# Optimization experiments

Measured on AMD Instinct MI355X. Metric: run time of the kernel, lower is better.

Reference implementation:

```python
import jax, jax.numpy as jnp
import numpy as np

DEPTH = 10
LEAF = 2 ** DEPTH          # 1024 leaves
NODE_NUM = 2 * LEAF - 1    # 2047
N = NODE_NUM + 1           # 2048 nodes incl. global node 0
ATTN = 4
D = 128
B = 8
L = 2


def _trace_children(ni):
    terms = []
    s, e = ni << 1, (ni << 1) | 1
    while s <= NODE_NUM and e <= NODE_NUM:
        terms.extend(range(s, e + 1))
        s <<= 1
        e = (e << 1) | 1
    return terms


def _trace_left(si):
    ni, cd, terms, stop = si + LEAF, DEPTH, [], False
    while not stop:
        cs = ni - ATTN + 1 - ((ni - ATTN + 1) & 1)
        stop = cs < 2 ** cd
        cs = max(2 ** cd, cs)
        terms.extend(range(cs, ni + 1))
        ni = (cs - 1) >> 1
        cd -= 1
    return terms


def _trace_right(ei):
    ni, cd, terms, stop = ei + LEAF, DEPTH, [], False
    while not stop:
        ce = ni + ATTN - 1 + ((ni - ATTN) & 1)
        stop = ce >= 2 ** (cd + 1)
        ce = min(2 ** (cd + 1) - 1, ce)
        terms.extend(range(ni, ce + 1))
        ni = (ce + 1) >> 1
        cd -= 1
    return terms


def _build_edges():
    src, dst = [], []
    for ni in range(1, NODE_NUM + 1):
        if ni < LEAF:
            t = _trace_children(ni)
        else:
            t = _trace_left(ni - LEAF) + _trace_right(ni - LEAF)
        src.extend(t)
        dst.extend([ni] * len(t))
    e = np.stack([np.asarray(src, np.int64), np.asarray(dst, np.int64)])  # [2, E]
    off = np.arange(B, dtype=np.int64) * N
    eb = (e[:, None, :] + off[None, :, None]).reshape(2, -1)  # batch-offset like _fetch_edge_data
    return eb.astype(np.int32)


def setup_inputs() -> dict:
    key = jax.random.key(0)
    k0, k1, k2 = jax.random.split(key, 3)
    s = 1.0 / np.sqrt(D)
    return {
        "elements": jax.random.normal(k0, (B, LEAF, D), jnp.float32),
        "ln_gamma": jnp.ones((L, D), jnp.float32),
        "ln_beta": jnp.zeros((L, D), jnp.float32),
        "w_nei": (jax.random.normal(k1, (L, D, D), jnp.float32) * s),
        "b_nei": jnp.zeros((L, D), jnp.float32),
        "w_root": (jax.random.normal(k2, (L, D, D), jnp.float32) * s),
        "edge_index": jnp.asarray(_build_edges()),
    }


def _sinusoid(pos, d):
    # ArbitraryPositionEncoder: sinusoidal encoding over (possibly negative) positions
    half = d // 2
    inv = jnp.exp(-jnp.arange(half, dtype=jnp.float32) * (np.log(10000.0) / half))
    ang = pos[:, None] * inv[None, :]  # [n, half]
    return jnp.stack([jnp.sin(ang), jnp.cos(ang)], -1).reshape(pos.shape[0], d)


def reference(elements, ln_gamma, ln_beta, w_nei, b_nei, w_root, edge_index):
    Bx, leaf, d = elements.shape
    depth = int(np.log2(leaf))
    # bottom-up tree compression (mean of two children)
    cur = elements
    levels = [cur]
    for _ in range(depth):
        cur = 0.5 * (cur[:, 0::2] + cur[:, 1::2])
        levels.append(cur)
    # node ordering: [global node 0 (=-1), root (level 0), ..., leaves (level depth)]
    node_feat = jnp.concatenate(
        [jnp.full((Bx, 1, d), -1.0, elements.dtype)] + levels[::-1], axis=1)  # [B, N, D]
    n = node_feat.shape[1]
    # positional encoding: vertical = floor(log2(idx)), horizontal = idx - 2^vertical
    idx = jnp.arange(n, dtype=jnp.float32)
    vpos = jnp.floor(jnp.log2(jnp.where(idx == 0, 0.5, idx)))
    hpos = idx - jnp.exp2(vpos)
    enc = jnp.concatenate([_sinusoid(hpos, d // 2), _sinusoid(vpos, d // 2)], -1)  # [N, D]
    x = (node_feat + enc[None]).reshape(Bx * n, d)
    src, dst = edge_index[0], edge_index[1]
    nseg = Bx * n
    deg = jnp.maximum(
        jax.ops.segment_sum(jnp.ones(src.shape, jnp.float32), dst, num_segments=nseg), 1.0)
    # DeepGCNLayer res+ blocks with SAGEConv (mean aggr)
    for l in range(ln_gamma.shape[0]):
        mu = jnp.mean(x, -1, keepdims=True)
        var = jnp.mean((x - mu) ** 2, -1, keepdims=True)
        h = (x - mu) * jax.lax.rsqrt(var + 1e-5) * ln_gamma[l] + ln_beta[l]
        h = jax.nn.gelu(h, approximate=False)
        agg = jax.ops.segment_sum(h[src], dst, num_segments=nseg) / deg[:, None]
        h = agg @ w_nei[l] + b_nei[l] + h @ w_root[l]
        x = x + h
    return x.reshape(Bx, n, d)
```

## Files before the change

### kernel.cpp

```cpp
#include <hip/hip_runtime.h>
#include <hip/hip_bf16.h>

#define LEAFN 1024
#define NN    2048
#define BATCH 8
#define DD    128
#define ROWS  (BATCH*NN)
#define AHS   384
#define NB    256
#define NT    512

#define LOG1E4_OVER_32 0.28782313662425575f

#define SLACK 9
#define CSTRIDE 136
#define AGGL_OFF 54672
#define RED_OFF  63376

typedef __bf16 bf16x8 __attribute__((ext_vector_type(8)));
typedef float  floatx4 __attribute__((ext_vector_type(4)));
typedef float  floatx2 __attribute__((ext_vector_type(2)));

__device__ __forceinline__ float bf2f(unsigned short u) {
  return __uint_as_float(((unsigned)u) << 16);
}
__device__ __forceinline__ unsigned short f2bf(float f) {
  unsigned u = __float_as_uint(f);
  u += 0x7FFFu + ((u >> 16) & 1u);
  return (unsigned short)(u >> 16);
}
__device__ __forceinline__ float gelu(float v) {
  return 0.5f * v * (1.0f + erff(v * 0.70710678118f));
}
__device__ __forceinline__ floatx2 bfpair(unsigned u) {
  floatx2 r;
  r[0] = __uint_as_float(u << 16);
  r[1] = __uint_as_float(u & 0xffff0000u);
  return r;
}

__device__ __forceinline__ float enc_val(int node, int d) {
  float hp, vp;
  if (node == 0) { hp = -0.5f; vp = -1.0f; }
  else {
    int v = 31 - __clz(node);
    hp = (float)(node - (1 << v));
    vp = (float)v;
  }
  float pos = (d < 64) ? hp : vp;
  int i = ((d < 64) ? d : (d - 64)) >> 1;
  float inv = __expf(-(float)i * LOG1E4_OVER_32);
  float ang = pos * inv;
  return (d & 1) ? __cosf(ang) : __sinf(ang);
}

__device__ __forceinline__ void win_cd(int jb, int cd, int& lo_, int& wd_) {
  int g0 = 1024 + jb * 32, g1 = g0 + 31;
  int a0 = g0 >> (10 - cd), a1 = g1 >> (10 - cd);
  int l = a0 - SLACK, h = a1 + SLACK;
  int lvlo = 1 << cd, lvhi = (2 << cd) - 1;
  lo_ = l < lvlo ? lvlo : l;
  int hh = h > lvhi ? lvhi : h;
  int w = hh - lo_ + 1;
  wd_ = w < 0 ? 0 : w;
}

__device__ __forceinline__ void gbarN(int* bar, int slot) {
  __syncthreads();
  if (threadIdx.x == 0) {
    int g = blockIdx.x & 7;
    int* base = bar + (slot * 8 + g) * 64;
    __threadfence();
    if (__hip_atomic_fetch_add(base, 1, __ATOMIC_RELAXED,
                               __HIP_MEMORY_SCOPE_AGENT) == 31)
      __hip_atomic_store(base + 32, 1, __ATOMIC_RELAXED,
                         __HIP_MEMORY_SCOPE_AGENT);
    while (!__hip_atomic_load(base + 32, __ATOMIC_RELAXED,
                              __HIP_MEMORY_SCOPE_AGENT))
      __builtin_amdgcn_s_sleep(1);
    __threadfence();
  }
  __syncthreads();
}

__device__ __forceinline__ void ph_tree(char* smemc, int b, int s,
                                        const float* __restrict__ elements,
                                        float* __restrict__ x,
                                        float* __restrict__ lvl4,
                                        unsigned short* __restrict__ ah,
                                        const float* __restrict__ gamma,
                                        const float* __restrict__ beta,
                                        float* __restrict__ sroot,
                                        float* xci, int* bar) {
  float* sm = (float*)smemc;
  int tid = threadIdx.x;
  const float4* src = (const float4*)(elements + (size_t)(b * LEAFN + s * 64) * DD);
  for (int i = tid; i < 2048; i += NT) {
    int f = i * 4;
    int j = f >> 7, d = f & 127;
    *(float4*)&sm[(63 + j) * DD + d] = src[i];
  }
  __syncthreads();
  for (int lv = 5; lv >= 0; --lv) {
    int nodes = 1 << lv;
    for (int idx = tid; idx < nodes * DD; idx += NT) {
      int k = nodes + (idx >> 7);
      int d = idx & 127;
      sm[(k - 1) * DD + d] = 0.5f * (sm[(2 * k - 1) * DD + d] + sm[(2 * k) * DD + d]);
    }
    __syncthreads();
  }
  if (tid < DD) lvl4[(b * 16 + s) * DD + tid] = sm[tid];
  __syncthreads();
  if (tid == 0) {
    __threadfence();
    __hip_atomic_store(bar + 1536 + b * 64 + s * 4, 1, __ATOMIC_RELAXED,
                       __HIP_MEMORY_SCOPE_AGENT);
  }
  for (int idx = tid; idx < 127 * DD; idx += NT) {
    int k = (idx >> 7) + 1;
    int d = idx & 127;
    int lv = 31 - __clz(k);
    int g = ((16 + s) << lv) | (k - (1 << lv));
    float xv = sm[idx] + enc_val(g, d);
    if (k >= 64) x[((size_t)(b * NN + g)) * DD + d] = xv;
    sm[idx] = xv;
  }
  __syncthreads();
  {
    int wave = tid >> 6, lane = tid & 63;
    int mt = wave >> 2, nq = wave & 3;
    int m = lane & 15, q = lane >> 4;
#pragma unroll
    for (int c = 0; c < 2; ++c)
#pragma unroll
      for (int ci = 0; ci < 2; ++ci)
#pragma unroll
        for (int r = 0; r < 4; ++r) {
          int t = c * 32 + mt * 16 + q * 4 + r;
          int k = (t == 63) ? 1 : t + 1;
          int d = (nq * 2 + ci) * 16 + m;
          xci[c * 8 + ci * 4 + r] = sm[(k - 1) * DD + d];
        }
  }
  __syncthreads();
  {
    int sub = tid & 7, dp = sub * 16;
    for (int rr = tid >> 3; rr < 127; rr += NT / 8) {
      float* rowp = &sm[rr * DD + dp];
      float4 q0 = *(float4*)rowp;
      float4 q1 = *(float4*)(rowp + 4);
      float4 q2 = *(float4*)(rowp + 8);
      float4 q3 = *(float4*)(rowp + 12);
      float v[16] = {q0.x, q0.y, q0.z, q0.w, q1.x, q1.y, q1.z, q1.w,
                     q2.x, q2.y, q2.z, q2.w, q3.x, q3.y, q3.z, q3.w};
      float s1 = 0.f, s2 = 0.f;
#pragma unroll
      for (int j = 0; j < 16; ++j) { s1 += v[j]; s2 += v[j] * v[j]; }
      s1 += __shfl_xor(s1, 1); s2 += __shfl_xor(s2, 1);
      s1 += __shfl_xor(s1, 2); s2 += __shfl_xor(s2, 2);
      s1 += __shfl_xor(s1, 4); s2 += __shfl_xor(s2, 4);
      float mu = s1 * (1.0f / 128.0f);
      float var = s2 * (1.0f / 128.0f) - mu * mu;
      float rinv = rsqrtf(var + 1e-5f);
      int k = rr + 1, lv = 31 - __clz(k);
      int g = ((16 + s) << lv) | (k - (1 << lv));
      __attribute__((aligned(16))) unsigned short o[16];
      float hv[16];
#pragma unroll
      for (int j = 0; j < 16; ++j) {
        hv[j] = gelu((v[j] - mu) * rinv * gamma[dp + j] + beta[dp + j]);
        o[j] = f2bf(hv[j]);
      }
      *(float4*)rowp        = make_float4(hv[0], hv[1], hv[2], hv[3]);
      *(float4*)(rowp + 4)  = make_float4(hv[4], hv[5], hv[6], hv[7]);
      *(float4*)(rowp + 8)  = make_float4(hv[8], hv[9], hv[10], hv[11]);
      *(float4*)(rowp + 12) = make_float4(hv[12], hv[13], hv[14], hv[15]);
      unsigned short* dst = &ah[(size_t)(b * NN + g) * AHS + 128 + dp];
      *(uint4*)&dst[0] = *(uint4*)&o[0];
      *(uint4*)&dst[8] = *(uint4*)&o[8];
    }
  }
  __syncthreads();
  for (int lv = 5; lv >= 0; --lv) {
    int nk = 1 << lv;
    float inv = 1.0f / (float)((1 << (7 - lv)) - 2);
    for (int idx = tid; idx < nk * DD; idx += NT) {
      int k = nk + (idx >> 7);
      int d = idx & 127;
      float S = sm[(2 * k - 1) * DD + d] + sm[(2 * k) * DD + d];
      if (lv < 5) S += sm[(4 * k - 1) * DD + d] + sm[(4 * k + 1) * DD + d];
      sm[(2 * k - 1) * DD + d] = S;
      int g = ((16 + s) << lv) | (k - nk);
      ah[(size_t)(b * NN + g) * AHS + d] = f2bf(S * inv);
    }
    __syncthreads();
  }
  if (tid < DD) sroot[(size_t)(b * 16 + s) * DD + tid] = sm[DD + tid];
}

__device__ __forceinline__ void ph_top(char* smemc, int b,
                                       const float* __restrict__ lvl4,
                                       unsigned short* __restrict__ ah,
                                       const float* __restrict__ gamma,
                                       const float* __restrict__ beta) {
  float (*xs)[DD] = (float(*)[DD])smemc;
  int tid = threadIdx.x;
  if (tid < 128) {
    int d = tid;
    float v[16];
    for (int j = 0; j < 16; ++j) v[j] = lvl4[(b * 16 + j) * DD + d];
    for (int j = 0; j < 8; ++j) v[j] = 0.5f * (v[2 * j] + v[2 * j + 1]);
    for (int j = 0; j < 8; ++j) xs[8 + j][d] = v[j] + enc_val(8 + j, d);
    for (int j = 0; j < 4; ++j) v[j] = 0.5f * (v[2 * j] + v[2 * j + 1]);
    for (int j = 0; j < 4; ++j) xs[4 + j][d] = v[j] + enc_val(4 + j, d);
    for (int j = 0; j < 2; ++j) v[j] = 0.5f * (v[2 * j] + v[2 * j + 1]);
    for (int j = 0; j < 2; ++j) xs[2 + j][d] = v[j] + enc_val(2 + j, d);
    v[0] = 0.5f * (v[0] + v[1]);
    xs[1][d] = v[0] + enc_val(1, d);
    xs[0][d] = -1.0f + enc_val(0, d);
  }
  __syncthreads();
  if (tid < 128) {
    int rr = tid >> 3, sub = tid & 7, dp = sub * 16;
    float w[16], s1 = 0.f, s2 = 0.f;
#pragma unroll
    for (int j = 0; j < 16; ++j) { w[j] = xs[rr][dp + j]; s1 += w[j]; s2 += w[j] * w[j]; }
    s1 += __shfl_xor(s1, 1); s2 += __shfl_xor(s2, 1);
    s1 += __shfl_xor(s1, 2); s2 += __shfl_xor(s2, 2);
    s1 += __shfl_xor(s1, 4); s2 += __shfl_xor(s2, 4);
    float mu = s1 * (1.0f / 128.0f);
    float var = s2 * (1.0f / 128.0f) - mu * mu;
    float rinv = rsqrtf(var + 1e-5f);
    __attribute__((aligned(16))) unsigned short o[16];
#pragma unroll
    for (int j = 0; j < 16; ++j)
      o[j] = f2bf(gelu((w[j] - mu) * rinv * gamma[dp + j] + beta[dp + j]));
    unsigned short* dst = &ah[(size_t)(b * NN + rr) * AHS + 128 + dp];
    *(uint4*)&dst[0] = *(uint4*)&o[0];
    *(uint4*)&dst[8] = *(uint4*)&o[8];
  }
  __syncthreads();
}

__device__ __forceinline__ void ph_aggsub(char* smemc, int b, int s,
                                          unsigned short* ah,
                                          float* __restrict__ sroot) {
  floatx4 (*S)[32] = (floatx4(*)[32])smemc;
  int tid = threadIdx.x;
  for (int idx = tid; idx < 32 * 32; idx += NT) {
    int k = 32 + (idx >> 5), q = idx & 31;
    int c = (16 + s) * 64 + (2 * k - 64);
    size_t a0 = (size_t)(b * NN + c) * AHS + 256 + q * 4;
    ushort4 u0 = *(const ushort4*)&ah[a0];
    ushort4 u1 = *(const ushort4*)&ah[a0 + AHS];
    floatx4 v;
    v[0] = bf2f(u0.x) + bf2f(u1.x);
    v[1] = bf2f(u0.y) + bf2f(u1.y);
    v[2] = bf2f(u0.z) + bf2f(u1.z);
    v[3] = bf2f(u0.w) + bf2f(u1.w);
    S[k][q] = v;
    int g = (16 + s) * 32 + (k - 32);
    int r = b * NN + g;
    ushort4 o;
    o.x = f2bf(v[0] * 0.5f); o.y = f2bf(v[1] * 0.5f);
    o.z = f2bf(v[2] * 0.5f); o.w = f2bf(v[3] * 0.5f);
    *(ushort4*)&ah[(size_t)r * AHS + q * 4] = o;
  }
  __syncthreads();
  for (int lv = 4; lv >= 0; --lv) {
    int nk = 1 << lv;
    float inv = 1.0f / (float)((1 << (7 - lv)) - 2);
    for (int idx = tid; idx < nk * 32; idx += NT) {
      int k = nk + (idx >> 5), q = idx & 31;
      int c = ((16 + s) << (lv + 1)) | (2 * k - 2 * nk);
      size_t a0 = (size_t)(b * NN + c) * AHS + 256 + q * 4;
      ushort4 u0 = *(const ushort4*)&ah[a0];
      ushort4 u1 = *(const ushort4*)&ah[a0 + AHS];
      floatx4 sc0 = S[2 * k][q], sc1 = S[2 * k + 1][q];
      floatx4 v;
      v[0] = bf2f(u0.x) + bf2f(u1.x) + sc0[0] + sc1[0];
      v[1] = bf2f(u0.y) + bf2f(u1.y) + sc0[1] + sc1[1];
      v[2] = bf2f(u0.z) + bf2f(u1.z) + sc0[2] + sc1[2];
      v[3] = bf2f(u0.w) + bf2f(u1.w) + sc0[3] + sc1[3];
      S[k][q] = v;
      int g = ((16 + s) << lv) | (k - nk);
      int r = b * NN + g;
      ushort4 o;
      o.x = f2bf(v[0] * inv); o.y = f2bf(v[1] * inv);
      o.z = f2bf(v[2] * inv); o.w = f2bf(v[3] * inv);
      *(ushort4*)&ah[(size_t)r * AHS + q * 4] = o;
    }
    __syncthreads();
  }
  for (int q = tid; q < 32; q += NT)
    ((floatx4*)sroot)[(size_t)(b * 16 + s) * 32 + q] = S[1][q];
}

__device__ __forceinline__ void ph_leafagg(char* smemc, int b, int jb,
                                           const int* __restrict__ srcv,
                                           const int* __restrict__ s0a,
                                           const int* __restrict__ s1a,
                                           const unsigned short* __restrict__ eoff,
                                           unsigned short* ah, int hoff) {
  unsigned short* cache = (unsigned short*)smemc;
  int tid = threadIdx.x;
  int lo[11], wd[11], off[11];
  int acc_off = 0;
#pragma unroll
  for (int cd = 10; cd >= 1; --cd) {
    win_cd(jb, cd, lo[cd], wd[cd]);
    off[cd] = acc_off;
    acc_off += wd[cd];
  }
#pragma unroll
  for (int cd = 10; cd >= 1; --cd) {
    int w = wd[cd];
    for (int t = tid; t < w * 16; t += NT) {
      int row = t >> 4, seg = t & 15;
      *(uint4*)&cache[(off[cd] + row) * CSTRIDE + seg * 8] =
          *(const uint4*)&ah[(size_t)(b * NN + lo[cd] + row) * AHS + hoff + seg * 8];
    }
  }
  __syncthreads();

  int leaf = tid >> 4, c = tid & 15;
  int r = b * NN + 1024 + jb * 32 + leaf;
  int e0 = s0a[r], e1 = s1a[r];
  int cb = c * 16;
  floatx2 a0 = {0.f, 0.f}, a1 = {0.f, 0.f}, a2 = {0.f, 0.f}, a3 = {0.f, 0.f};
  auto one = [&](int ei) {
    unsigned o = eoff[ei];
    uint4 u;
    if (o != 0xFFFFu)
      u = *(const uint4*)(smemc + o + cb);
    else {
      int g = srcv[ei] - b * NN;
      u = *(const uint4*)&ah[(size_t)(b * NN + g) * AHS + hoff + c * 8];
    }
    a0 += bfpair(u.x); a1 += bfpair(u.y); a2 += bfpair(u.z); a3 += bfpair(u.w);
  };
  int e = e0;
  for (; e + 4 <= e1; e += 4) {
    unsigned o0 = eoff[e], o1 = eoff[e + 1], o2 = eoff[e + 2], o3 = eoff[e + 3];
    if (!((((o0 + 1) | (o1 + 1) | (o2 + 1) | (o3 + 1)) >> 16))) {
      uint4 u0 = *(const uint4*)(smemc + o0 + cb);
      uint4 u1 = *(const uint4*)(smemc + o1 + cb);
      uint4 u2 = *(const uint4*)(smemc + o2 + cb);
      uint4 u3 = *(const uint4*)(smemc + o3 + cb);
      a0 += bfpair(u0.x); a1 += bfpair(u0.y); a2 += bfpair(u0.z); a3 += bfpair(u0.w);
      a0 += bfpair(u1.x); a1 += bfpair(u1.y); a2 += bfpair(u1.z); a3 += bfpair(u1.w);
      a0 += bfpair(u2.x); a1 += bfpair(u2.y); a2 += bfpair(u2.z); a3 += bfpair(u2.w);
      a0 += bfpair(u3.x); a1 += bfpair(u3.y); a2 += bfpair(u3.z); a3 += bfpair(u3.w);
    } else {
      one(e); one(e + 1); one(e + 2); one(e + 3);
    }
  }
  for (; e < e1; ++e) one(e);
  float inv = 1.0f / (float)max(e1 - e0, 1);
  unsigned short* aggl = (unsigned short*)(smemc + AGGL_OFF);
  __attribute__((aligned(16))) unsigned short o[8];
  o[0] = f2bf(a0[0] * inv); o[1] = f2bf(a0[1] * inv);
  o[2] = f2bf(a1[0] * inv); o[3] = f2bf(a1[1] * inv);
  o[4] = f2bf(a2[0] * inv); o[5] = f2bf(a2[1] * inv);
  o[6] = f2bf(a3[0] * inv); o[7] = f2bf(a3[1] * inv);
  *(uint4*)&aggl[leaf * CSTRIDE + c * 8] = *(uint4*)&o[0];
}

__device__ __forceinline__ void ph_topfin(int b,
                                          const float* __restrict__ sroot,
                                          unsigned short* ah, int hoff) {
  int d = threadIdx.x;
  float S16[16], h16[16], Sv[16];
#pragma unroll
  for (int j = 0; j < 16; ++j) S16[j] = sroot[(size_t)(b * 16 + j) * DD + d];
#pragma unroll
  for (int j = 0; j < 16; ++j)
    h16[j] = bf2f(ah[(size_t)(b * NN + 16 + j) * AHS + hoff + d]);
#pragma unroll
  for (int k = 8; k < 16; ++k)
    Sv[k] = h16[2 * k - 16] + h16[2 * k - 15] + S16[2 * k - 16] + S16[2 * k - 15];
#pragma unroll
  for (int k = 7; k >= 1; --k)
    Sv[k] = bf2f(ah[(size_t)(b * NN + 2 * k) * AHS + hoff + d]) +
            bf2f(ah[(size_t)(b * NN + 2 * k + 1) * AHS + hoff + d]) +
            Sv[2 * k] + Sv[2 * k + 1];
#pragma unroll
  for (int k = 1; k < 16; ++k) {
    int dv = 31 - __clz(k);
    float inv = 1.0f / (float)((1 << (11 - dv)) - 2);
    ah[(size_t)(b * NN + k) * AHS + d] = f2bf(Sv[k] * inv);
  }
  ah[(size_t)(b * NN) * AHS + d] = f2bf(0.0f);
}

__device__ __forceinline__ void ph_gemm32(char* redc, const unsigned short* aggl,
                                          int rowbase, unsigned short* ah,
                                          const unsigned short* __restrict__ wfl,
                                          const float* __restrict__ bn,
                                          float* __restrict__ x, int hoff_in,
                                          const float* __restrict__ gamma,
                                          const float* __restrict__ beta,
                                          float* xc, int first_layer) {
  int wave = threadIdx.x >> 6, lane = threadIdx.x & 63;
  int mt = wave >> 2, nq = wave & 3;
  int r0 = rowbase + mt * 16;
  int m = lane & 15, q = lane >> 4;
  const unsigned short* arow = ah + (size_t)(r0 + m) * AHS + q * 8;
  const bf16x8* B = (const bf16x8*)wfl + lane;
  floatx4 acc[2];
  acc[0] = (floatx4){0.f, 0.f, 0.f, 0.f};
  acc[1] = (floatx4){0.f, 0.f, 0.f, 0.f};
#pragma unroll
  for (int kc = 0; kc < 8; ++kc) {
    bf16x8 a0;
    if (kc < 4)
      a0 = *(const bf16x8*)&aggl[(mt * 16 + m) * CSTRIDE + kc * 32 + q * 8];
    else
      a0 = *(const bf16x8*)(arow + hoff_in + (kc - 4) * 32);
#pragma unroll
    for (int ci = 0; ci < 2; ++ci) {
      bf16x8 bb = B[(kc * 8 + nq * 2 + ci) * 64];
      acc[ci] = __builtin_amdgcn_mfma_f32_16x16x32_bf16(a0, bb, acc[ci], 0, 0, 0);
    }
  }
  if (first_layer) {
    float s1[4] = {0.f, 0.f, 0.f, 0.f}, s2[4] = {0.f, 0.f, 0.f, 0.f};
#pragma unroll
    for (int ci = 0; ci < 2; ++ci) {
      int col = (nq * 2 + ci) * 16 + m;
      float bias = bn[col];
#pragma unroll
      for (int r = 0; r < 4; ++r) {
        int row = r0 + q * 4 + r;
        float v = x[(size_t)row * DD + col] + acc[ci][r] + bias;
        xc[ci * 4 + r] = v;
        s1[r] += v; s2[r] += v * v;
      }
    }
#pragma unroll
    for (int r = 0; r < 4; ++r) {
      s1[r] += __shfl_xor(s1[r], 1); s2[r] += __shfl_xor(s2[r], 1);
      s1[r] += __shfl_xor(s1[r], 2); s2[r] += __shfl_xor(s2[r], 2);
      s1[r] += __shfl_xor(s1[r], 4); s2[r] += __shfl_xor(s2[r], 4);
      s1[r] += __shfl_xor(s1[r], 8); s2[r] += __shfl_xor(s2[r], 8);
    }
    float* red = (float*)redc;
    int rl = mt * 16 + q * 4;
    __syncthreads();
    if (m == 0) {
#pragma unroll
      for (int r = 0; r < 4; ++r) {
        red[(rl + r) * 4 + nq] = s1[r];
        red[128 + (rl + r) * 4 + nq] = s2[r];
      }
    }
    __syncthreads();
    float mu[4], rv[4];
#pragma unroll
    for (int r = 0; r < 4; ++r) {
      float t1 = red[(rl + r) * 4] + red[(rl + r) * 4 + 1] +
                 red[(rl + r) * 4 + 2] + red[(rl + r) * 4 + 3];
      float t2 = red[128 + (rl + r) * 4] + red[128 + (rl + r) * 4 + 1] +
                 red[128 + (rl + r) * 4 + 2] + red[128 + (rl + r) * 4 + 3];
      mu[r] = t1 * (1.0f / 128.0f);
      float var = t2 * (1.0f / 128.0f) - mu[r] * mu[r];
      rv[r] = rsqrtf(var + 1e-5f);
    }
#pragma unroll
    for (int ci = 0; ci < 2; ++ci) {
      int col = (nq * 2 + ci) * 16 + m;
      float gm = gamma[col], bt = beta[col];
#pragma unroll
      for (int r = 0; r < 4; ++r) {
        int row = r0 + q * 4 + r;
        float hh = gelu((xc[ci * 4 + r] - mu[r]) * rv[r] * gm + bt);
        ah[(size_t)row * AHS + 256 + col] = f2bf(hh);
      }
    }
  } else {
#pragma unroll
    for (int ci = 0; ci < 2; ++ci) {
      int col = (nq * 2 + ci) * 16 + m;
      float bias = bn[col];
#pragma unroll
      for (int r = 0; r < 4; ++r) {
        int row = r0 + q * 4 + r;
        x[(size_t)row * DD + col] = xc[ci * 4 + r] + acc[ci][r] + bias;
      }
    }
  }
}

__device__ __forceinline__ void ph_gemm32s(char* redc, int b, int sb, int tbase,
                                           unsigned short* ah,
                                           const unsigned short* __restrict__ wfl,
                                           const float* __restrict__ bn,
                                           float* __restrict__ x, int hoff_in,
                                           const float* __restrict__ gamma,
                                           const float* __restrict__ beta,
                                           float* xc, int first_layer) {
  int wave = threadIdx.x >> 6, lane = threadIdx.x & 63;
  int mt = wave >> 2, nq = wave & 3;
  int m = lane & 15, q = lane >> 4;
  int tA = tbase + mt * 16 + m;
  int kA = (tA == 63) ? 1 : tA + 1;
  int lvA = 31 - __clz(kA);
  int rowA = b * NN + (((16 + sb) << lvA) | (kA - (1 << lvA)));
  int rowO[4];
#pragma unroll
  for (int r = 0; r < 4; ++r) {
    int t = tbase + mt * 16 + q * 4 + r;
    int k = (t == 63) ? 1 : t + 1;
    int lv = 31 - __clz(k);
    rowO[r] = b * NN + (((16 + sb) << lv) | (k - (1 << lv)));
  }
  const unsigned short* arow = ah + (size_t)rowA * AHS + q * 8;
  const bf16x8* B = (const bf16x8*)wfl + lane;
  floatx4 acc[2];
  acc[0] = (floatx4){0.f, 0.f, 0.f, 0.f};
  acc[1] = (floatx4){0.f, 0.f, 0.f, 0.f};
#pragma unroll
  for (int kc = 0; kc < 8; ++kc) {
    int koff = (kc < 4) ? kc * 32 : hoff_in + (kc - 4) * 32;
    bf16x8 a0 = *(const bf16x8*)(arow + koff);
#pragma unroll
    for (int ci = 0; ci < 2; ++ci) {
      bf16x8 bb = B[(kc * 8 + nq * 2 + ci) * 64];
      acc[ci] = __builtin_amdgcn_mfma_f32_16x16x32_bf16(a0, bb, acc[ci], 0, 0, 0);
    }
  }
  if (first_layer) {
    float s1[4] = {0.f, 0.f, 0.f, 0.f}, s2[4] = {0.f, 0.f, 0.f, 0.f};
#pragma unroll
    for (int ci = 0; ci < 2; ++ci) {
      int col = (nq * 2 + ci) * 16 + m;
      float bias = bn[col];
#pragma unroll
      for (int r = 0; r < 4; ++r) {
        float v = xc[ci * 4 + r] + acc[ci][r] + bias;
        xc[ci * 4 + r] = v;
        s1[r] += v; s2[r] += v * v;
      }
    }
#pragma unroll
    for (int r = 0; r < 4; ++r) {
      s1[r] += __shfl_xor(s1[r], 1); s2[r] += __shfl_xor(s2[r], 1);
      s1[r] += __shfl_xor(s1[r], 2); s2[r] += __shfl_xor(s2[r], 2);
      s1[r] += __shfl_xor(s1[r], 4); s2[r] += __shfl_xor(s2[r], 4);
      s1[r] += __shfl_xor(s1[r], 8); s2[r] += __shfl_xor(s2[r], 8);
    }
    float* red = (float*)redc;
    int rl = mt * 16 + q * 4;
    __syncthreads();
    if (m == 0) {
#pragma unroll
      for (int r = 0; r < 4; ++r) {
        red[(rl + r) * 4 + nq] = s1[r];
        red[128 + (rl + r) * 4 + nq] = s2[r];
      }
    }
    __syncthreads();
    float mu[4], rv[4];
#pragma unroll
    for (int r = 0; r < 4; ++r) {
      float t1 = red[(rl + r) * 4] + red[(rl + r) * 4 + 1] +
                 red[(rl + r) * 4 + 2] + red[(rl + r) * 4 + 3];
      float t2 = red[128 + (rl + r) * 4] + red[128 + (rl + r) * 4 + 1] +
                 red[128 + (rl + r) * 4 + 2] + red[128 + (rl + r) * 4 + 3];
      mu[r] = t1 * (1.0f / 128.0f);
      float var = t2 * (1.0f / 128.0f) - mu[r] * mu[r];
      rv[r] = rsqrtf(var + 1e-5f);
    }
#pragma unroll
    for (int ci = 0; ci < 2; ++ci) {
      int col = (nq * 2 + ci) * 16 + m;
      float gm = gamma[col], bt = beta[col];
#pragma unroll
      for (int r = 0; r < 4; ++r) {
        float hh = gelu((xc[ci * 4 + r] - mu[r]) * rv[r] * gm + bt);
        ah[(size_t)rowO[r] * AHS + 256 + col] = f2bf(hh);
      }
    }
  } else {
#pragma unroll
    for (int ci = 0; ci < 2; ++ci) {
      int col = (nq * 2 + ci) * 16 + m;
      float bias = bn[col];
#pragma unroll
      for (int r = 0; r < 4; ++r)
        x[(size_t)rowO[r] * DD + col] = xc[ci * 4 + r] + acc[ci][r] + bias;
    }
  }
}

__device__ __forceinline__ void ph_gemm16t(char* redc, int b,
                                           unsigned short* ah,
                                           const unsigned short* __restrict__ wfl,
                                           const float* __restrict__ bn,
                                           float* __restrict__ x, int hoff_in,
                                           const float* __restrict__ gamma,
                                           const float* __restrict__ beta,
                                           float* xc, int first_layer) {
  int ct = threadIdx.x >> 6, lane = threadIdx.x & 63;
  int m = lane & 15, q = lane >> 4;
  const unsigned short* arow = ah + (size_t)(b * NN + m) * AHS + q * 8;
  const bf16x8* B = (const bf16x8*)wfl + lane;
  floatx4 acc = (floatx4){0.f, 0.f, 0.f, 0.f};
#pragma unroll
  for (int kc = 0; kc < 8; ++kc) {
    int koff = (kc < 4) ? kc * 32 : hoff_in + (kc - 4) * 32;
    bf16x8 a0 = *(const bf16x8*)(arow + koff);
    bf16x8 bb = B[(kc * 8 + ct) * 64];
    acc = __builtin_amdgcn_mfma_f32_16x16x32_bf16(a0, bb, acc, 0, 0, 0);
  }
  int col = ct * 16 + m;
  float bias = bn[col];
  if (first_layer) {
    float s1[4], s2[4];
#pragma unroll
    for (int r = 0; r < 4; ++r) {
      float v = xc[r] + acc[r] + bias;
      xc[r] = v; s1[r] = v; s2[r] = v * v;
    }
#pragma unroll
    for (int r = 0; r < 4; ++r) {
      s1[r] += __shfl_xor(s1[r], 1); s2[r] += __shfl_xor(s2[r], 1);
      s1[r] += __shfl_xor(s1[r], 2); s2[r] += __shfl_xor(s2[r], 2);
      s1[r] += __shfl_xor(s1[r], 4); s2[r] += __shfl_xor(s2[r], 4);
      s1[r] += __shfl_xor(s1[r], 8); s2[r] += __shfl_xor(s2[r], 8);
    }
    float* red = (float*)redc;
    __syncthreads();
    if (m == 0) {
#pragma unroll
      for (int r = 0; r < 4; ++r) {
        red[(q * 4 + r) * 8 + ct] = s1[r];
        red[128 + (q * 4 + r) * 8 + ct] = s2[r];
      }
    }
    __syncthreads();
#pragma unroll
    for (int r = 0; r < 4; ++r) {
      float t1 = 0.f, t2 = 0.f;
#pragma unroll
      for (int j = 0; j < 8; ++j) {
        t1 += red[(q * 4 + r) * 8 + j];
        t2 += red[128 + (q * 4 + r) * 8 + j];
      }
      float mu = t1 * (1.0f / 128.0f);
      float var = t2 * (1.0f / 128.0f) - mu * mu;
      float rv = rsqrtf(var + 1e-5f);
      float hh = gelu((xc[r] - mu) * rv * gamma[col] + beta[col]);
      ah[(size_t)(b * NN + q * 4 + r) * AHS + 256 + col] = f2bf(hh);
    }
  } else {
#pragma unroll
    for (int r = 0; r < 4; ++r)
      x[(size_t)(b * NN + q * 4 + r) * DD + col] = xc[r] + acc[r] + bias;
  }
}

__global__ __launch_bounds__(NT, 1) void k_mega(
    const float* __restrict__ elements, const float* __restrict__ ln_gamma,
    const float* __restrict__ ln_beta, const float* __restrict__ w_nei,
    const float* __restrict__ b_nei, const float* __restrict__ w_root,
    const int* __restrict__ srcv, const int* __restrict__ dstv, int E,
    float* __restrict__ x, int* s0a, int* s1a, float* lvl4, float* sroot,
    unsigned short* wf, unsigned short* ah, unsigned short* eoff, int* bar) {
  __shared__ __align__(16) char smem[65536];
  int bid = blockIdx.x, tid = threadIdx.x;
  int b = bid & 7, gb = bid >> 3;
  int Eb = E >> 3;
  unsigned short* wfg = wf + (size_t)b * 65536;
  float xcl[8], xci[16], xct[4];

  if (gb < 16) {
    ph_tree(smem, b, gb, elements, x, lvl4, ah, ln_gamma, ln_beta, sroot, xci, bar);
  } else if (gb < 24) {
    int base = b * Eb;
    for (int i = base + (gb - 16) * NT + tid; i < base + Eb; i += 8 * NT) {
      int dv = dstv[i];
      if (i == 0 || dstv[i - 1] != dv) s0a[dv] = i;
      if (i == base + Eb - 1 || dstv[i + 1] != dv) s1a[dv] = i + 1;
    }
    for (int i = base + (gb - 16) * NT + tid; i < base + Eb; i += 8 * NT) {
      int dl = dstv[i] - b * NN - 1024;
      unsigned short ov = 0xFFFFu;
      if (dl >= 0) {
        int jb2 = dl >> 5;
        int g = srcv[i] - b * NN;
        int lv = 31 - __clz(g);
        int acc2 = 0;
#pragma unroll
        for (int cd = 10; cd >= 1; --cd) {
          int lo_, wd_;
          win_cd(jb2, cd, lo_, wd_);
          if (cd == lv) {
            int idx = g - lo_;
            if ((unsigned)idx < (unsigned)wd_)
              ov = (unsigned short)((acc2 + idx) * (2 * CSTRIDE));
          }
          acc2 += wd_;
        }
      }
      eoff[i] = ov;
    }
    if (gb == 16) {
      if (tid < 16) {
        while (!__hip_atomic_load(bar + 1536 + b * 64 + tid * 4, __ATOMIC_RELAXED,
                                  __HIP_MEMORY_SCOPE_AGENT))
          __builtin_amdgcn_s_sleep(1);
        __threadfence();
      }
      __syncthreads();
      ph_top(smem, b, lvl4, ah, ln_gamma, ln_beta);
      {
        int wv = tid >> 6, ln = tid & 63, m_ = ln & 15, q_ = ln >> 4;
        float (*xs)[DD] = (float(*)[DD])smem;
#pragma unroll
        for (int r = 0; r < 4; ++r) xct[r] = xs[q_ * 4 + r][wv * 16 + m_];
      }
    }
  } else {
    int gi = (gb - 24) * NT + tid;
    int lane = gi & 63, ct = (gi >> 6) & 7, kc = gi >> 9;
    int n = ct * 16 + (lane & 15);
    int k = kc * 32 + (lane >> 4) * 8;
    int kk = k & 127;
#pragma unroll
    for (int l = 0; l < 2; ++l) {
      const float* w = (k < 128) ? (w_nei + (size_t)l * DD * DD)
                                 : (w_root + (size_t)l * DD * DD);
      unsigned short* o = wfg + (size_t)l * 32768 + (size_t)gi * 8;
#pragma unroll
      for (int j = 0; j < 8; ++j) o[j] = f2bf(w[(size_t)(kk + j) * DD + n]);
    }
  }
  gbarN(bar, 0);

  if (gb == 16) {
    if (tid < 128) ph_topfin(b, sroot, ah, 128);
    __syncthreads();
    ph_gemm16t(smem + RED_OFF, b, ah, wfg, b_nei, x, 128,
               ln_gamma + DD, ln_beta + DD, xct, 1);
    __syncthreads();
  }
  ph_leafagg(smem, b, gb, srcv, s0a, s1a, eoff, ah, 128);
  __syncthreads();
  ph_gemm32(smem + RED_OFF, (const unsigned short*)(smem + AGGL_OFF),
            b * NN + 1024 + gb * 32, ah, wfg, b_nei, x, 128,
            ln_gamma + DD, ln_beta + DD, xcl, 1);
  if (gb < 16) {
    ph_gemm32s(smem + RED_OFF, b, gb, 0, ah, wfg, b_nei, x, 128,
               ln_gamma + DD, ln_beta + DD, xci, 1);
    ph_gemm32s(smem + RED_OFF, b, gb, 32, ah, wfg, b_nei, x, 128,
               ln_gamma + DD, ln_beta + DD, xci + 8, 1);
  }
  gbarN(bar, 1);

  if (gb < 16) {
    ph_aggsub(smem, b, gb, ah, sroot);
    __syncthreads();
    if (tid == 0) {
      __threadfence();
      __hip_atomic_store(bar + 1024 + b * 64 + gb * 4, 1, __ATOMIC_RELAXED,
                         __HIP_MEMORY_SCOPE_AGENT);
    }
  }
  ph_leafagg(smem, b, gb, srcv, s0a, s1a, eoff, ah, 256);
  __syncthreads();
  ph_gemm32(smem + RED_OFF, (const unsigned short*)(smem + AGGL_OFF),
            b * NN + 1024 + gb * 32, ah, wfg + 32768, b_nei + DD,
            x, 256, ln_gamma, ln_beta, xcl, 0);
  if (gb < 16) {
    ph_gemm32s(smem + RED_OFF, b, gb, 0, ah, wfg + 32768, b_nei + DD, x, 256,
               ln_gamma, ln_beta, xci, 0);
    ph_gemm32s(smem + RED_OFF, b, gb, 32, ah, wfg + 32768, b_nei + DD, x, 256,
               ln_gamma, ln_beta, xci + 8, 0);
  } else if (gb == 16) {
    if (tid < 16) {
      while (!__hip_atomic_load(bar + 1024 + b * 64 + tid * 4, __ATOMIC_RELAXED,
                                __HIP_MEMORY_SCOPE_AGENT))
        __builtin_amdgcn_s_sleep(1);
      __threadfence();
    }
    __syncthreads();
    if (tid < 128) ph_topfin(b, sroot, ah, 256);
    __syncthreads();
    ph_gemm16t(smem + RED_OFF, b, ah, wfg + 32768, b_nei + DD, x, 256,
               ln_gamma, ln_beta, xct, 0);
  }
}

extern "C" void kernel_launch(void* const* d_in, const int* in_sizes, int n_in,
                              void* d_out, int out_size, void* d_ws, size_t ws_size,
                              hipStream_t stream) {
  const float* elements = (const float*)d_in[0];
  const float* ln_gamma = (const float*)d_in[1];
  const float* ln_beta  = (const float*)d_in[2];
  const float* w_nei    = (const float*)d_in[3];
  const float* b_nei    = (const float*)d_in[4];
  const float* w_root   = (const float*)d_in[5];
  const int*   edge     = (const int*)d_in[6];
  int E = in_sizes[6] / 2;
  const int* srcv = edge;
  const int* dstv = edge + E;
  float* x = (float*)d_out;

  char* ws = (char*)d_ws;
  int*            bar   = (int*)ws;
  int*            s0    = (int*)(ws + 65536);
  int*            s1    = (int*)(ws + 131072);
  float*          lvl4  = (float*)(ws + 196608);
  float*          sroot = (float*)(ws + 262144);
  unsigned short* wf    = (unsigned short*)(ws + 327680);
  unsigned short* ah    = (unsigned short*)(ws + 327680 + 1048576);
  unsigned short* eoff  = (unsigned short*)(ws + 327680 + 1048576 + 12582912);

  hipMemsetAsync(bar, 0, 8192, stream);
  k_mega<<<dim3(NB), dim3(NT), 0, stream>>>(
      elements, ln_gamma, ln_beta, w_nei, b_nei, w_root,
      srcv, dstv, E, x, s0, s1, lvl4, sroot, wf, ah, eoff, bar);
}
```

Before: 175.0 us.

## Double block threads to 1024 and split leaf edge aggregation across two half-groups

Raises threads per block from 512 to 1024 in the persistent mega-kernel. Leaf aggregation now gives each leaf two 16-lane groups that each sum half of its edge list and combine the halves with a shuffle. The MFMA GEMM phases keep only the first 8 waves active and guard the extra waves. The aim is more latency hiding in the gather-heavy aggregation, at the risk of halving the register budget per thread and adding idle waves that still pay at every block barrier.

New measurement: 169.0 us. 3.5% less time.

```diff
diff --git a/kernel.cpp b/kernel.cpp
--- a/kernel.cpp
+++ b/kernel.cpp
@@ -8,7 +8,7 @@
 #define ROWS  (BATCH*NN)
 #define AHS   384
 #define NB    256
-#define NT    512
+#define NT    1024
 
 #define LOG1E4_OVER_32 0.28782313662425575f
 
@@ -129,19 +129,21 @@
   __syncthreads();
   {
     int wave = tid >> 6, lane = tid & 63;
-    int mt = wave >> 2, nq = wave & 3;
-    int m = lane & 15, q = lane >> 4;
-#pragma unroll
-    for (int c = 0; c < 2; ++c)
-#pragma unroll
-      for (int ci = 0; ci < 2; ++ci)
-#pragma unroll
-        for (int r = 0; r < 4; ++r) {
-          int t = c * 32 + mt * 16 + q * 4 + r;
-          int k = (t == 63) ? 1 : t + 1;
-          int d = (nq * 2 + ci) * 16 + m;
-          xci[c * 8 + ci * 4 + r] = sm[(k - 1) * DD + d];
-        }
+    if (wave < 8) {
+      int mt = wave >> 2, nq = wave & 3;
+      int m = lane & 15, q = lane >> 4;
+#pragma unroll
+      for (int c = 0; c < 2; ++c)
+#pragma unroll
+        for (int ci = 0; ci < 2; ++ci)
+#pragma unroll
+          for (int r = 0; r < 4; ++r) {
+            int t = c * 32 + mt * 16 + q * 4 + r;
+            int k = (t == 63) ? 1 : t + 1;
+            int d = (nq * 2 + ci) * 16 + m;
+            xci[c * 8 + ci * 4 + r] = sm[(k - 1) * DD + d];
+          }
+    }
   }
   __syncthreads();
   {
@@ -324,9 +326,13 @@
   }
   __syncthreads();
 
-  int leaf = tid >> 4, c = tid & 15;
+  int leaf = tid >> 5, half = (tid >> 4) & 1, c = tid & 15;
   int r = b * NN + 1024 + jb * 32 + leaf;
   int e0 = s0a[r], e1 = s1a[r];
+  int n = e1 - e0;
+  int mid = e0 + (n >> 1);
+  int ebeg = half ? mid : e0;
+  int eend = half ? e1 : mid;
   int cb = c * 16;
   floatx2 a0 = {0.f, 0.f}, a1 = {0.f, 0.f}, a2 = {0.f, 0.f}, a3 = {0.f, 0.f};
   auto one = [&](int ei) {
@@ -340,8 +346,8 @@
     }
     a0 += bfpair(u.x); a1 += bfpair(u.y); a2 += bfpair(u.z); a3 += bfpair(u.w);
   };
-  int e = e0;
-  for (; e + 4 <= e1; e += 4) {
+  int e = ebeg;
+  for (; e + 4 <= eend; e += 4) {
     unsigned o0 = eoff[e], o1 = eoff[e + 1], o2 = eoff[e + 2], o3 = eoff[e + 3];
     if (!((((o0 + 1) | (o1 + 1) | (o2 + 1) | (o3 + 1)) >> 16))) {
       uint4 u0 = *(const uint4*)(smemc + o0 + cb);
@@ -356,15 +362,21 @@
       one(e); one(e + 1); one(e + 2); one(e + 3);
     }
   }
-  for (; e < e1; ++e) one(e);
-  float inv = 1.0f / (float)max(e1 - e0, 1);
-  unsigned short* aggl = (unsigned short*)(smemc + AGGL_OFF);
-  __attribute__((aligned(16))) unsigned short o[8];
-  o[0] = f2bf(a0[0] * inv); o[1] = f2bf(a0[1] * inv);
-  o[2] = f2bf(a1[0] * inv); o[3] = f2bf(a1[1] * inv);
-  o[4] = f2bf(a2[0] * inv); o[5] = f2bf(a2[1] * inv);
-  o[6] = f2bf(a3[0] * inv); o[7] = f2bf(a3[1] * inv);
-  *(uint4*)&aggl[leaf * CSTRIDE + c * 8] = *(uint4*)&o[0];
+  for (; e < eend; ++e) one(e);
+  a0[0] += __shfl_xor(a0[0], 16); a0[1] += __shfl_xor(a0[1], 16);
+  a1[0] += __shfl_xor(a1[0], 16); a1[1] += __shfl_xor(a1[1], 16);
+  a2[0] += __shfl_xor(a2[0], 16); a2[1] += __shfl_xor(a2[1], 16);
+  a3[0] += __shfl_xor(a3[0], 16); a3[1] += __shfl_xor(a3[1], 16);
+  if (!half) {
+    float inv = 1.0f / (float)max(n, 1);
+    unsigned short* aggl = (unsigned short*)(smemc + AGGL_OFF);
+    __attribute__((aligned(16))) unsigned short o[8];
+    o[0] = f2bf(a0[0] * inv); o[1] = f2bf(a0[1] * inv);
+    o[2] = f2bf(a1[0] * inv); o[3] = f2bf(a1[1] * inv);
+    o[4] = f2bf(a2[0] * inv); o[5] = f2bf(a2[1] * inv);
+    o[6] = f2bf(a3[0] * inv); o[7] = f2bf(a3[1] * inv);
+    *(uint4*)&aggl[leaf * CSTRIDE + c * 8] = *(uint4*)&o[0];
+  }
 }
 
 __device__ __forceinline__ void ph_topfin(int b,
@@ -403,52 +415,57 @@
                                           const float* __restrict__ beta,
                                           float* xc, int first_layer) {
   int wave = threadIdx.x >> 6, lane = threadIdx.x & 63;
-  int mt = wave >> 2, nq = wave & 3;
+  bool act = wave < 8;
+  int mt = (wave & 7) >> 2, nq = wave & 3;
   int r0 = rowbase + mt * 16;
   int m = lane & 15, q = lane >> 4;
-  const unsigned short* arow = ah + (size_t)(r0 + m) * AHS + q * 8;
-  const bf16x8* B = (const bf16x8*)wfl + lane;
   floatx4 acc[2];
   acc[0] = (floatx4){0.f, 0.f, 0.f, 0.f};
   acc[1] = (floatx4){0.f, 0.f, 0.f, 0.f};
-#pragma unroll
-  for (int kc = 0; kc < 8; ++kc) {
-    bf16x8 a0;
-    if (kc < 4)
-      a0 = *(const bf16x8*)&aggl[(mt * 16 + m) * CSTRIDE + kc * 32 + q * 8];
-    else
-      a0 = *(const bf16x8*)(arow + hoff_in + (kc - 4) * 32);
-#pragma unroll
-    for (int ci = 0; ci < 2; ++ci) {
-      bf16x8 bb = B[(kc * 8 + nq * 2 + ci) * 64];
-      acc[ci] = __builtin_amdgcn_mfma_f32_16x16x32_bf16(a0, bb, acc[ci], 0, 0, 0);
+  if (act) {
+    const unsigned short* arow = ah + (size_t)(r0 + m) * AHS + q * 8;
+    const bf16x8* B = (const bf16x8*)wfl + lane;
+#pragma unroll
+    for (int kc = 0; kc < 8; ++kc) {
+      bf16x8 a0;
+      if (kc < 4)
+        a0 = *(const bf16x8*)&aggl[(mt * 16 + m) * CSTRIDE + kc * 32 + q * 8];
+      else
+        a0 = *(const bf16x8*)(arow + hoff_in + (kc - 4) * 32);
+#pragma unroll
+      for (int ci = 0; ci < 2; ++ci) {
+        bf16x8 bb = B[(kc * 8 + nq * 2 + ci) * 64];
+        acc[ci] = __builtin_amdgcn_mfma_f32_16x16x32_bf16(a0, bb, acc[ci], 0, 0, 0);
+      }
     }
   }
   if (first_layer) {
     float s1[4] = {0.f, 0.f, 0.f, 0.f}, s2[4] = {0.f, 0.f, 0.f, 0.f};
-#pragma unroll
-    for (int ci = 0; ci < 2; ++ci) {
-      int col = (nq * 2 + ci) * 16 + m;
-      float bias = bn[col];
-#pragma unroll
-      for (int r = 0; r < 4; ++r) {
-        int row = r0 + q * 4 + r;
-        float v = x[(size_t)row * DD + col] + acc[ci][r] + bias;
-        xc[ci * 4 + r] = v;
-        s1[r] += v; s2[r] += v * v;
-      }
-    }
-#pragma unroll
-    for (int r = 0; r < 4; ++r) {
-      s1[r] += __shfl_xor(s1[r], 1); s2[r] += __shfl_xor(s2[r], 1);
-      s1[r] += __shfl_xor(s1[r], 2); s2[r] += __shfl_xor(s2[r], 2);
-      s1[r] += __shfl_xor(s1[r], 4); s2[r] += __shfl_xor(s2[r], 4);
-      s1[r] += __shfl_xor(s1[r], 8); s2[r] += __shfl_xor(s2[r], 8);
+    if (act) {
+#pragma unroll
+      for (int ci = 0; ci < 2; ++ci) {
+        int col = (nq * 2 + ci) * 16 + m;
+        float bias = bn[col];
+#pragma unroll
+        for (int r = 0; r < 4; ++r) {
+          int row = r0 + q * 4 + r;
+          float v = x[(size_t)row * DD + col] + acc[ci][r] + bias;
+          xc[ci * 4 + r] = v;
+          s1[r] += v; s2[r] += v * v;
+        }
+      }
+#pragma unroll
+      for (int r = 0; r < 4; ++r) {
+        s1[r] += __shfl_xor(s1[r], 1); s2[r] += __shfl_xor(s2[r], 1);
+        s1[r] += __shfl_xor(s1[r], 2); s2[r] += __shfl_xor(s2[r], 2);
+        s1[r] += __shfl_xor(s1[r], 4); s2[r] += __shfl_xor(s2[r], 4);
+        s1[r] += __shfl_xor(s1[r], 8); s2[r] += __shfl_xor(s2[r], 8);
+      }
     }
     float* red = (float*)redc;
     int rl = mt * 16 + q * 4;
     __syncthreads();
-    if (m == 0) {
+    if (act && m == 0) {
 #pragma unroll
       for (int r = 0; r < 4; ++r) {
         red[(rl + r) * 4 + nq] = s1[r];
@@ -456,37 +473,41 @@
       }
     }
     __syncthreads();
-    float mu[4], rv[4];
-#pragma unroll
-    for (int r = 0; r < 4; ++r) {
-      float t1 = red[(rl + r) * 4] + red[(rl + r) * 4 + 1] +
-                 red[(rl + r) * 4 + 2] + red[(rl + r) * 4 + 3];
-      float t2 = red[128 + (rl + r) * 4] + red[128 + (rl + r) * 4 + 1] +
-                 red[128 + (rl + r) * 4 + 2] + red[128 + (rl + r) * 4 + 3];
-      mu[r] = t1 * (1.0f / 128.0f);
-      float var = t2 * (1.0f / 128.0f) - mu[r] * mu[r];
-      rv[r] = rsqrtf(var + 1e-5f);
-    }
-#pragma unroll
-    for (int ci = 0; ci < 2; ++ci) {
-      int col = (nq * 2 + ci) * 16 + m;
-      float gm = gamma[col], bt = beta[col];
-#pragma unroll
-      for (int r = 0; r < 4; ++r) {
-        int row = r0 + q * 4 + r;
-        float hh = gelu((xc[ci * 4 + r] - mu[r]) * rv[r] * gm + bt);
-        ah[(size_t)row * AHS + 256 + col] = f2bf(hh);
+    if (act) {
+      float mu[4], rv[4];
+#pragma unroll
+      for (int r = 0; r < 4; ++r) {
+        float t1 = red[(rl + r) * 4] + red[(rl + r) * 4 + 1] +
+                   red[(rl + r) * 4 + 2] + red[(rl + r) * 4 + 3];
+        float t2 = red[128 + (rl + r) * 4] + red[128 + (rl + r) * 4 + 1] +
+                   red[128 + (rl + r) * 4 + 2] + red[128 + (rl + r) * 4 + 3];
+        mu[r] = t1 * (1.0f / 128.0f);
+        float var = t2 * (1.0f / 128.0f) - mu[r] * mu[r];
+        rv[r] = rsqrtf(var + 1e-5f);
+      }
+#pragma unroll
+      for (int ci = 0; ci < 2; ++ci) {
+        int col = (nq * 2 + ci) * 16 + m;
+        float gm = gamma[col], bt = beta[col];
+#pragma unroll
+        for (int r = 0; r < 4; ++r) {
+          int row = r0 + q * 4 + r;
+          float hh = gelu((xc[ci * 4 + r] - mu[r]) * rv[r] * gm + bt);
+          ah[(size_t)row * AHS + 256 + col] = f2bf(hh);
+        }
       }
     }
   } else {
-#pragma unroll
-    for (int ci = 0; ci < 2; ++ci) {
-      int col = (nq * 2 + ci) * 16 + m;
-      float bias = bn[col];
-#pragma unroll
-      for (int r = 0; r < 4; ++r) {
-        int row = r0 + q * 4 + r;
-        x[(size_t)row * DD + col] = xc[ci * 4 + r] + acc[ci][r] + bias;
+    if (act) {
+#pragma unroll
+      for (int ci = 0; ci < 2; ++ci) {
+        int col = (nq * 2 + ci) * 16 + m;
+        float bias = bn[col];
+#pragma unroll
+        for (int r = 0; r < 4; ++r) {
+          int row = r0 + q * 4 + r;
+          x[(size_t)row * DD + col] = xc[ci * 4 + r] + acc[ci][r] + bias;
+        }
       }
     }
   }
@@ -501,7 +522,8 @@
                                            const float* __restrict__ beta,
                                            float* xc, int first_layer) {
   int wave = threadIdx.x >> 6, lane = threadIdx.x & 63;
-  int mt = wave >> 2, nq = wave & 3;
+  bool act = wave < 8;
+  int mt = (wave & 7) >> 2, nq = wave & 3;
   int m = lane & 15, q = lane >> 4;
   int tA = tbase + mt * 16 + m;
   int kA = (tA == 63) ? 1 : tA + 1;
@@ -515,45 +537,49 @@
     int lv = 31 - __clz(k);
     rowO[r] = b * NN + (((16 + sb) << lv) | (k - (1 << lv)));
   }
-  const unsigned short* arow = ah + (size_t)rowA * AHS + q * 8;
-  const bf16x8* B = (const bf16x8*)wfl + lane;
   floatx4 acc[2];
   acc[0] = (floatx4){0.f, 0.f, 0.f, 0.f};
   acc[1] = (floatx4){0.f, 0.f, 0.f, 0.f};
-#pragma unroll
-  for (int kc = 0; kc < 8; ++kc) {
-    int koff = (kc < 4) ? kc * 32 : hoff_in + (kc - 4) * 32;
-    bf16x8 a0 = *(const bf16x8*)(arow + koff);
-#pragma unroll
-    for (int ci = 0; ci < 2; ++ci) {
-      bf16x8 bb = B[(kc * 8 + nq * 2 + ci) * 64];
-      acc[ci] = __builtin_amdgcn_mfma_f32_16x16x32_bf16(a0, bb, acc[ci], 0, 0, 0);
+  if (act) {
+    const unsigned short* arow = ah + (size_t)rowA * AHS + q * 8;
+    const bf16x8* B = (const bf16x8*)wfl + lane;
+#pragma unroll
+    for (int kc = 0; kc < 8; ++kc) {
+      int koff = (kc < 4) ? kc * 32 : hoff_in + (kc - 4) * 32;
+      bf16x8 a0 = *(const bf16x8*)(arow + koff);
+#pragma unroll
+      for (int ci = 0; ci < 2; ++ci) {
+        bf16x8 bb = B[(kc * 8 + nq * 2 + ci) * 64];
+        acc[ci] = __builtin_amdgcn_mfma_f32_16x16x32_bf16(a0, bb, acc[ci], 0, 0, 0);
+      }
     }
   }
   if (first_layer) {
     float s1[4] = {0.f, 0.f, 0.f, 0.f}, s2[4] = {0.f, 0.f, 0.f, 0.f};
-#pragma unroll
-    for (int ci = 0; ci < 2; ++ci) {
-      int col = (nq * 2 + ci) * 16 + m;
-      float bias = bn[col];
-#pragma unroll
-      for (int r = 0; r < 4; ++r) {
-        float v = xc[ci * 4 + r] + acc[ci][r] + bias;
-        xc[ci * 4 + r] = v;
-        s1[r] += v; s2[r] += v * v;
-      }
-    }
-#pragma unroll
-    for (int r = 0; r < 4; ++r) {
-      s1[r] += __shfl_xor(s1[r], 1); s2[r] += __shfl_xor(s2[r], 1);
-      s1[r] += __shfl_xor(s1[r], 2); s2[r] += __shfl_xor(s2[r], 2);
-      s1[r] += __shfl_xor(s1[r], 4); s2[r] += __shfl_xor(s2[r], 4);
-      s1[r] += __shfl_xor(s1[r], 8); s2[r] += __shfl_xor(s2[r], 8);
+    if (act) {
+#pragma unroll
+      for (int ci = 0; ci < 2; ++ci) {
+        int col = (nq * 2 + ci) * 16 + m;
+        float bias = bn[col];
+#pragma unroll
+        for (int r = 0; r < 4; ++r) {
+          float v = xc[ci * 4 + r] + acc[ci][r] + bias;
+          xc[ci * 4 + r] = v;
+          s1[r] += v; s2[r] += v * v;
+        }
+      }
+#pragma unroll
+      for (int r = 0; r < 4; ++r) {
+        s1[r] += __shfl_xor(s1[r], 1); s2[r] += __shfl_xor(s2[r], 1);
+        s1[r] += __shfl_xor(s1[r], 2); s2[r] += __shfl_xor(s2[r], 2);
+        s1[r] += __shfl_xor(s1[r], 4); s2[r] += __shfl_xor(s2[r], 4);
+        s1[r] += __shfl_xor(s1[r], 8); s2[r] += __shfl_xor(s2[r], 8);
+      }
     }
     float* red = (float*)redc;
     int rl = mt * 16 + q * 4;
     __syncthreads();
-    if (m == 0) {
+    if (act && m == 0) {
 #pragma unroll
       for (int r = 0; r < 4; ++r) {
         red[(rl + r) * 4 + nq] = s1[r];
@@ -561,35 +587,39 @@
       }
     }
     __syncthreads();
-    float mu[4], rv[4];
-#pragma unroll
-    for (int r = 0; r < 4; ++r) {
-      float t1 = red[(rl + r) * 4] + red[(rl + r) * 4 + 1] +
-                 red[(rl + r) * 4 + 2] + red[(rl + r) * 4 + 3];
-      float t2 = red[128 + (rl + r) * 4] + red[128 + (rl + r) * 4 + 1] +
-                 red[128 + (rl + r) * 4 + 2] + red[128 + (rl + r) * 4 + 3];
-      mu[r] = t1 * (1.0f / 128.0f);
-      float var = t2 * (1.0f / 128.0f) - mu[r] * mu[r];
-      rv[r] = rsqrtf(var + 1e-5f);
-    }
-#pragma unroll
-    for (int ci = 0; ci < 2; ++ci) {
-      int col = (nq * 2 + ci) * 16 + m;
-      float gm = gamma[col], bt = beta[col];
-#pragma unroll
-      for (int r = 0; r < 4; ++r) {
-        float hh = gelu((xc[ci * 4 + r] - mu[r]) * rv[r] * gm + bt);
-        ah[(size_t)rowO[r] * AHS + 256 + col] = f2bf(hh);
+    if (act) {
+      float mu[4], rv[4];
+#pragma unroll
+      for (int r = 0; r < 4; ++r) {
+        float t1 = red[(rl + r) * 4] + red[(rl + r) * 4 + 1] +
+                   red[(rl + r) * 4 + 2] + red[(rl + r) * 4 + 3];
+        float t2 = red[128 + (rl + r) * 4] + red[128 + (rl + r) * 4 + 1] +
+                   red[128 + (rl + r) * 4 + 2] + red[128 + (rl + r) * 4 + 3];
+        mu[r] = t1 * (1.0f / 128.0f);
+        float var = t2 * (1.0f / 128.0f) - mu[r] * mu[r];
+        rv[r] = rsqrtf(var + 1e-5f);
+      }
+#pragma unroll
+      for (int ci = 0; ci < 2; ++ci) {
+        int col = (nq * 2 + ci) * 16 + m;
+        float gm = gamma[col], bt = beta[col];
+#pragma unroll
+        for (int r = 0; r < 4; ++r) {
+          float hh = gelu((xc[ci * 4 + r] - mu[r]) * rv[r] * gm + bt);
+          ah[(size_t)rowO[r] * AHS + 256 + col] = f2bf(hh);
+        }
       }
     }
   } else {
-#pragma unroll
-    for (int ci = 0; ci < 2; ++ci) {
-      int col = (nq * 2 + ci) * 16 + m;
-      float bias = bn[col];
-#pragma unroll
-      for (int r = 0; r < 4; ++r)
-        x[(size_t)rowO[r] * DD + col] = xc[ci * 4 + r] + acc[ci][r] + bias;
+    if (act) {
+#pragma unroll
+      for (int ci = 0; ci < 2; ++ci) {
+        int col = (nq * 2 + ci) * 16 + m;
+        float bias = bn[col];
+#pragma unroll
+        for (int r = 0; r < 4; ++r)
+          x[(size_t)rowO[r] * DD + col] = xc[ci * 4 + r] + acc[ci][r] + bias;
+      }
     }
   }
 }
@@ -603,36 +633,41 @@
                                            const float* __restrict__ beta,
                                            float* xc, int first_layer) {
   int ct = threadIdx.x >> 6, lane = threadIdx.x & 63;
+  bool act = ct < 8;
   int m = lane & 15, q = lane >> 4;
-  const unsigned short* arow = ah + (size_t)(b * NN + m) * AHS + q * 8;
-  const bf16x8* B = (const bf16x8*)wfl + lane;
   floatx4 acc = (floatx4){0.f, 0.f, 0.f, 0.f};
-#pragma unroll
-  for (int kc = 0; kc < 8; ++kc) {
-    int koff = (kc < 4) ? kc * 32 : hoff_in + (kc - 4) * 32;
-    bf16x8 a0 = *(const bf16x8*)(arow + koff);
-    bf16x8 bb = B[(kc * 8 + ct) * 64];
-    acc = __builtin_amdgcn_mfma_f32_16x16x32_bf16(a0, bb, acc, 0, 0, 0);
-  }
-  int col = ct * 16 + m;
-  float bias = bn[col];
+  int col = (ct & 7) * 16 + m;
+  if (act) {
+    const unsigned short* arow = ah + (size_t)(b * NN + m) * AHS + q * 8;
+    const bf16x8* B = (const bf16x8*)wfl + lane;
+#pragma unroll
+    for (int kc = 0; kc < 8; ++kc) {
+      int koff = (kc < 4) ? kc * 32 : hoff_in + (kc - 4) * 32;
+      bf16x8 a0 = *(const bf16x8*)(arow + koff);
+      bf16x8 bb = B[(kc * 8 + ct) * 64];
+      acc = __builtin_amdgcn_mfma_f32_16x16x32_bf16(a0, bb, acc, 0, 0, 0);
+    }
+  }
   if (first_layer) {
-    float s1[4], s2[4];
-#pragma unroll
-    for (int r = 0; r < 4; ++r) {
-      float v = xc[r] + acc[r] + bias;
-      xc[r] = v; s1[r] = v; s2[r] = v * v;
-    }
-#pragma unroll
-    for (int r = 0; r < 4; ++r) {
-      s1[r] += __shfl_xor(s1[r], 1); s2[r] += __shfl_xor(s2[r], 1);
-      s1[r] += __shfl_xor(s1[r], 2); s2[r] += __shfl_xor(s2[r], 2);
-      s1[r] += __shfl_xor(s1[r], 4); s2[r] += __shfl_xor(s2[r], 4);
-      s1[r] += __shfl_xor(s1[r], 8); s2[r] += __shfl_xor(s2[r], 8);
+    float s1[4] = {0.f, 0.f, 0.f, 0.f}, s2[4] = {0.f, 0.f, 0.f, 0.f};
+    float bias = act ? bn[col] : 0.f;
+    if (act) {
+#pragma unroll
+      for (int r = 0; r < 4; ++r) {
+        float v = xc[r] + acc[r] + bias;
+        xc[r] = v; s1[r] = v; s2[r] = v * v;
+      }
+#pragma unroll
+      for (int r = 0; r < 4; ++r) {
+        s1[r] += __shfl_xor(s1[r], 1); s2[r] += __shfl_xor(s2[r], 1);
+        s1[r] += __shfl_xor(s1[r], 2); s2[r] += __shfl_xor(s2[r], 2);
+        s1[r] += __shfl_xor(s1[r], 4); s2[r] += __shfl_xor(s2[r], 4);
+        s1[r] += __shfl_xor(s1[r], 8); s2[r] += __shfl_xor(s2[r], 8);
+      }
     }
     float* red = (float*)redc;
     __syncthreads();
-    if (m == 0) {
+    if (act && m == 0) {
 #pragma unroll
       for (int r = 0; r < 4; ++r) {
         red[(q * 4 + r) * 8 + ct] = s1[r];
@@ -640,24 +675,29 @@
       }
     }
     __syncthreads();
-#pragma unroll
-    for (int r = 0; r < 4; ++r) {
-      float t1 = 0.f, t2 = 0.f;
-#pragma unroll
-      for (int j = 0; j < 8; ++j) {
-        t1 += red[(q * 4 + r) * 8 + j];
-        t2 += red[128 + (q * 4 + r) * 8 + j];
-      }
-      float mu = t1 * (1.0f / 128.0f);
-      float var = t2 * (1.0f / 128.0f) - mu * mu;
-      float rv = rsqrtf(var + 1e-5f);
-      float hh = gelu((xc[r] - mu) * rv * gamma[col] + beta[col]);
-      ah[(size_t)(b * NN + q * 4 + r) * AHS + 256 + col] = f2bf(hh);
+    if (act) {
+#pragma unroll
+      for (int r = 0; r < 4; ++r) {
+        float t1 = 0.f, t2 = 0.f;
+#pragma unroll
+        for (int j = 0; j < 8; ++j) {
+          t1 += red[(q * 4 + r) * 8 + j];
+          t2 += red[128 + (q * 4 + r) * 8 + j];
+        }
+        float mu = t1 * (1.0f / 128.0f);
+        float var = t2 * (1.0f / 128.0f) - mu * mu;
+        float rv = rsqrtf(var + 1e-5f);
+        float hh = gelu((xc[r] - mu) * rv * gamma[col] + beta[col]);
+        ah[(size_t)(b * NN + q * 4 + r) * AHS + 256 + col] = f2bf(hh);
+      }
     }
   } else {
-#pragma unroll
-    for (int r = 0; r < 4; ++r)
-      x[(size_t)(b * NN + q * 4 + r) * DD + col] = xc[r] + acc[r] + bias;
+    if (act) {
+      float bias = bn[col];
+#pragma unroll
+      for (int r = 0; r < 4; ++r)
+        x[(size_t)(b * NN + q * 4 + r) * DD + col] = xc[r] + acc[r] + bias;
+    }
   }
 }
 
@@ -717,24 +757,28 @@
       ph_top(smem, b, lvl4, ah, ln_gamma, ln_beta);
       {
         int wv = tid >> 6, ln = tid & 63, m_ = ln & 15, q_ = ln >> 4;
-        float (*xs)[DD] = (float(*)[DD])smem;
-#pragma unroll
-        for (int r = 0; r < 4; ++r) xct[r] = xs[q_ * 4 + r][wv * 16 + m_];
+        if (wv < 8) {
+          float (*xs)[DD] = (float(*)[DD])smem;
+#pragma unroll
+          for (int r = 0; r < 4; ++r) xct[r] = xs[q_ * 4 + r][wv * 16 + m_];
+        }
       }
     }
   } else {
     int gi = (gb - 24) * NT + tid;
-    int lane = gi & 63, ct = (gi >> 6) & 7, kc = gi >> 9;
-    int n = ct * 16 + (lane & 15);
-    int k = kc * 32 + (lane >> 4) * 8;
-    int kk = k & 127;
-#pragma unroll
-    for (int l = 0; l < 2; ++l) {
-      const float* w = (k < 128) ? (w_nei + (size_t)l * DD * DD)
-                                 : (w_root + (size_t)l * DD * DD);
-      unsigned short* o = wfg + (size_t)l * 32768 + (size_t)gi * 8;
-#pragma unroll
-      for (int j = 0; j < 8; ++j) o[j] = f2bf(w[(size_t)(kk + j) * DD + n]);
+    if (gi < 4096) {
+      int lane = gi & 63, ct = (gi >> 6) & 7, kc = gi >> 9;
+      int n = ct * 16 + (lane & 15);
+      int k = kc * 32 + (lane >> 4) * 8;
+      int kk = k & 127;
+#pragma unroll
+      for (int l = 0; l < 2; ++l) {
+        const float* w = (k < 128) ? (w_nei + (size_t)l * DD * DD)
+                                   : (w_root + (size_t)l * DD * DD);
+        unsigned short* o = wfg + (size_t)l * 32768 + (size_t)gi * 8;
+#pragma unroll
+        for (int j = 0; j < 8; ++j) o[j] = f2bf(w[(size_t)(kk + j) * DD + n]);
+      }
     }
   }
   gbarN(bar, 0);
```
